# Optimization experiments

Hardware: AMD Instinct MI355X
Metric: run time of the kernel (lower is better)

The kernel has to match this reference:

```python
import jax, jax.numpy as jnp
import numpy as np

TAU = 2.0      # LIFNode default tau
VTH = 1.0      # v_threshold
ALPHA = 2.0    # ATan surrogate alpha
EPS = 1e-5     # BatchNorm eps
SCALE = 0.125  # hardcoded attention scale
HEADS = 8

@jax.custom_vjp
def atan_spike(x):
    return (x >= 0.0).astype(x.dtype)

def _atan_fwd(x):
    return atan_spike(x), x

def _atan_bwd(x, g):
    sg = (ALPHA / 2.0) / (1.0 + (jnp.pi / 2.0 * ALPHA * x) ** 2)
    return (g * sg,)

atan_spike.defvjp(_atan_fwd, _atan_bwd)

def lif(x_seq):
    # multi-step LIF: v' = v + (x - v)/tau ; spike = H(v'-1) ; hard reset to 0 (detach_reset)
    def step(v, x):
        v = v + (x - v) / TAU
        s = atan_spike(v - VTH)
        v = v * (1.0 - jax.lax.stop_gradient(s))
        return v, s
    _, spikes = jax.lax.scan(step, jnp.zeros_like(x_seq[0]), x_seq)
    return spikes

def bn(x, gamma, beta, mean, var):
    # inference-mode BatchNorm1d over channel axis 2 of [T,B,C,N]
    inv = gamma / jnp.sqrt(var + EPS)
    return x * inv[None, None, :, None] + (beta - mean * inv)[None, None, :, None]

def setup_inputs() -> dict:
    key = jax.random.key(0)
    ks = jax.random.split(key, 24)
    T, B, C, H, W = 4, 8, 512, 32, 32
    inp = {"x": jax.random.normal(ks[0], (T, B, C, H, W), dtype=jnp.float32)}
    i = 1
    for p in ("q", "k", "v", "proj"):
        inp[p + "_w"] = jax.random.normal(ks[i], (C, C), dtype=jnp.float32) / np.sqrt(C); i += 1
        inp[p + "_gamma"] = jax.random.uniform(ks[i], (C,), minval=0.5, maxval=1.5, dtype=jnp.float32); i += 1
        inp[p + "_beta"] = 0.1 * jax.random.normal(ks[i], (C,), dtype=jnp.float32); i += 1
        inp[p + "_mean"] = 0.1 * jax.random.normal(ks[i], (C,), dtype=jnp.float32); i += 1
        inp[p + "_var"] = jax.random.uniform(ks[i], (C,), minval=0.5, maxval=1.5, dtype=jnp.float32); i += 1
    inp["proj_b"] = 0.1 * jax.random.normal(ks[i], (C,), dtype=jnp.float32)
    return inp

def reference(x, q_w, q_gamma, q_beta, q_mean, q_var,
              k_w, k_gamma, k_beta, k_mean, k_var,
              v_w, v_gamma, v_beta, v_mean, v_var,
              proj_w, proj_gamma, proj_beta, proj_mean, proj_var, proj_b):
    T, B, C, H, W = x.shape
    N = H * W
    d = C // HEADS
    s = lif(x).reshape(T, B, C, N)  # proj_lif then flatten HW

    def branch(w, g, b, m, v_):
        y = jnp.einsum('oc,tbcn->tbon', w, s)  # conv1x1 == channel GEMM
        y = lif(bn(y, g, b, m, v_))
        # [T,B,C,N] -> [T,B,h,N,d]
        return y.reshape(T, B, HEADS, d, N).transpose(0, 1, 2, 4, 3)

    q = branch(q_w, q_gamma, q_beta, q_mean, q_var)
    k = branch(k_w, k_gamma, k_beta, k_mean, k_var)
    v = branch(v_w, v_gamma, v_beta, v_mean, v_var)

    kv = jnp.einsum('tbhnd,tbhne->tbhde', k, v)          # k^T v : [T,B,h,d,d]
    att = jnp.einsum('tbhnd,tbhde->tbhne', q, kv) * SCALE  # [T,B,h,N,d]
    att = att.transpose(0, 1, 2, 4, 3).reshape(T, B, C, N)
    a = lif(att)

    y = jnp.einsum('oc,tbcn->tbon', proj_w, a) + proj_b[None, None, :, None]
    y = bn(y, proj_gamma, proj_beta, proj_mean, proj_var)
    return y.reshape(T, B, C, H, W)
```

## Files before the change

### kernel.cpp

```cpp
#include <hip/hip_runtime.h>
#include <cstdint>
#include <cstddef>

typedef unsigned short u16;
typedef __attribute__((ext_vector_type(8))) short sh8;
typedef __attribute__((ext_vector_type(8))) _Float16 hf8;
typedef __attribute__((ext_vector_type(4))) float f4;

#define MFMA16B(a, b, c) __builtin_amdgcn_mfma_f32_16x16x32_bf16((a), (b), (c), 0, 0, 0)
#define MFMA16H(a, b, c) __builtin_amdgcn_mfma_f32_16x16x32_f16((a), (b), (c), 0, 0, 0)

__device__ __forceinline__ u16 f2bf(float f) {
  union { float f; uint32_t u; } v; v.f = f;
  uint32_t u = v.u;
  uint32_t lsb = (u >> 16) & 1u;
  return (u16)((u + 0x7fffu + lsb) >> 16);
}
__device__ __forceinline__ float bf2f(u16 h) {
  union { uint32_t u; float f; } v; v.u = ((uint32_t)h) << 16;
  return v.f;
}

__device__ __forceinline__ void aload16(const void* g, void* l) {
  __builtin_amdgcn_global_load_lds(
      (const __attribute__((address_space(1))) uint32_t*)g,
      (__attribute__((address_space(3))) uint32_t*)l, 16, 0, 0);
}

__global__ void prep_weights(const float* __restrict__ qw, const float* __restrict__ kw,
                             const float* __restrict__ vw, const float* __restrict__ pw,
                             u16* __restrict__ w2qkv, u16* __restrict__ w2p) {
  #pragma clang fp contract(off)
  int row = blockIdx.x;
  const float* src;
  u16* dst;
  int M, m;
  if (row < 1536) {
    int br = row >> 9;
    src = (br == 0 ? qw : (br == 1 ? kw : vw)) + (size_t)(row & 511) * 512;
    dst = w2qkv; M = 1536; m = row;
  } else {
    src = pw + (size_t)(row - 1536) * 512;
    dst = w2p; M = 512; m = row - 1536;
  }
  for (int c = threadIdx.x; c < 512; c += 256) {
    float w = src[c];
    _Float16 h0 = (_Float16)w;
    float r1 = w - (float)h0;
    _Float16 h1 = (_Float16)r1;
    union { _Float16 h; u16 u; } u0, u1;
    u0.h = h0; u1.h = h1;
    dst[(size_t)m * 512 + c] = u0.u;
    dst[(size_t)(M + m) * 512 + c] = u1.u;
  }
}

__global__ void bn_prep(const float* __restrict__ g, const float* __restrict__ be,
                        const float* __restrict__ mu, const float* __restrict__ va,
                        float* __restrict__ inv, float* __restrict__ add) {
  #pragma clang fp contract(off)
  int i = blockIdx.x * 256 + threadIdx.x;
  if (i < 512) {
    float iv = g[i] / sqrtf(va[i] + 1e-5f);
    inv[i] = iv;
    add[i] = be[i] - mu[i] * iv;
  }
}

__global__ __launch_bounds__(256) void lif0(const float* __restrict__ x, u16* __restrict__ sT) {
  #pragma clang fp contract(off)
  __shared__ u16 st[64 * 80];
  const int tid = threadIdx.x;
  const int n0 = blockIdx.x * 64;
  const int c0 = blockIdx.y * 64;
  const int b = blockIdx.z;
  const int cl = tid >> 2;
  const int ns = (tid & 3) * 16;
  const int nr = tid >> 2;
  const int cs = (tid & 3) * 16;
  float vv[16];
#pragma unroll
  for (int i = 0; i < 16; i++) vv[i] = 0.f;
  for (int t = 0; t < 4; ++t) {
    const float* xp = x + ((size_t)((t * 8 + b) * 512 + c0 + cl)) * 1024 + n0 + ns;
#pragma unroll
    for (int q = 0; q < 4; ++q) {
      f4 xv = *(const f4*)(xp + q * 4);
#pragma unroll
      for (int j = 0; j < 4; ++j) {
        int i = q * 4 + j;
        float v2 = vv[i] + (xv[j] - vv[i]) * 0.5f;
        int spk = (v2 - 1.0f >= 0.0f);
        st[(ns + i) * 80 + cl] = spk ? (u16)0x3C00 : (u16)0;
        vv[i] = spk ? 0.0f : v2;
      }
    }
    __syncthreads();
    u16* gp = sT + ((size_t)((t * 8 + b) * 1024 + n0 + nr)) * 512 + c0 + cs;
    *(sh8*)(gp) = *(const sh8*)&st[nr * 80 + cs];
    *(sh8*)(gp + 8) = *(const sh8*)&st[nr * 80 + cs + 8];
    __syncthreads();
  }
}

__global__ __launch_bounds__(256, 2) void qkv_gemm(
    const u16* __restrict__ w2, const u16* __restrict__ sT,
    const float* __restrict__ inv4, const float* __restrict__ add4,
    u16* __restrict__ qs, u16* __restrict__ ks, u16* __restrict__ vs) {
  #pragma clang fp contract(off)
  __shared__ u16 lA[2 * 128 * 32];
  __shared__ u16 lB[128 * 32];
  const int tid = threadIdx.x;
  const int m0 = blockIdx.x * 128;
  const int n0 = blockIdx.y * 128;
  const int b = blockIdx.z;
  const int branch = m0 >> 9;
  const int oc0 = m0 & 511;
  u16* dst = branch == 0 ? qs : (branch == 1 ? ks : vs);
  const int lane = tid & 63, wv = tid >> 6;
  const int l15 = lane & 15, l4 = lane >> 4;
  const int wm = wv >> 1, wn = wv & 1;
  const int rA = tid >> 2;
  const int kswz = (((tid & 3) ^ ((tid >> 3) & 3)) * 8);
  const int sA = (l4 ^ ((l15 >> 1) & 3)) * 8;

  size_t aoff[4];
#pragma unroll
  for (int c = 0; c < 4; ++c) {
    int rf = c * 64 + rA;
    int sp = rf >> 7, r = rf & 127;
    aoff[c] = (size_t)(sp * 1536 + m0 + r) * 512 + kswz;
  }
  size_t boff[2];
#pragma unroll
  for (int c = 0; c < 2; ++c) boff[c] = (size_t)(c * 64 + rA) * 512 + kswz;

  const f4 fz = {0.f, 0.f, 0.f, 0.f};
  f4 vst[4][4];
#pragma unroll
  for (int i = 0; i < 4; i++)
#pragma unroll
    for (int j = 0; j < 4; j++) vst[i][j] = fz;

  for (int t = 0; t < 4; ++t) {
    f4 acc[4][4];
#pragma unroll
    for (int i = 0; i < 4; i++)
#pragma unroll
      for (int j = 0; j < 4; j++) acc[i][j] = fz;
    const u16* sTt = sT + ((size_t)((t * 8 + b) * 1024 + n0)) * 512;

    for (int k0 = 0; k0 < 512; k0 += 32) {
#pragma unroll
      for (int c = 0; c < 4; ++c)
        aload16(w2 + aoff[c] + k0, &lA[c * 2048 + tid * 8]);
#pragma unroll
      for (int c = 0; c < 2; ++c)
        aload16(sTt + boff[c] + k0, &lB[c * 2048 + tid * 8]);
      __syncthreads();
      hf8 bfr[4];
#pragma unroll
      for (int nf = 0; nf < 4; ++nf)
        bfr[nf] = *(const hf8*)&lB[(wn * 64 + nf * 16 + l15) * 32 + sA];
#pragma unroll
      for (int sp = 0; sp < 2; ++sp) {
#pragma unroll
        for (int mf = 0; mf < 4; ++mf) {
          hf8 afr = *(const hf8*)&lA[sp * 4096 + (wm * 64 + mf * 16 + l15) * 32 + sA];
#pragma unroll
          for (int nf = 0; nf < 4; ++nf) acc[mf][nf] = MFMA16H(afr, bfr[nf], acc[mf][nf]);
        }
      }
      __syncthreads();
    }
#pragma unroll
    for (int mf = 0; mf < 4; ++mf) {
#pragma unroll
      for (int r = 0; r < 4; ++r) {
        int oc = oc0 + wm * 64 + mf * 16 + l4 * 4 + r;
        float iv = inv4[branch * 512 + oc];
        float ad = add4[branch * 512 + oc];
        size_t rowbase = ((size_t)((t * 8 + b) * 512 + oc)) * 1024 + n0;
#pragma unroll
        for (int nf = 0; nf < 4; ++nf) {
          float z = acc[mf][nf][r] * iv + ad;
          float v2 = vst[mf][nf][r];
          v2 = v2 + (z - v2) * 0.5f;
          int spk = (v2 - 1.0f >= 0.0f);
          vst[mf][nf][r] = spk ? 0.0f : v2;
          dst[rowbase + wn * 64 + nf * 16 + l15] = spk ? (u16)0x3F80 : (u16)0;
        }
      }
    }
  }
}

__global__ __launch_bounds__(256) void kv_gemm(const u16* __restrict__ ks,
                                               const u16* __restrict__ vs,
                                               float* __restrict__ kvp) {
  const int tbh = blockIdx.x;
  const int kc = blockIdx.y;
  const int tid = threadIdx.x;
  const int wv = tid >> 6, lane = tid & 63, l15 = lane & 15, l4 = lane >> 4;
  const size_t cb = ((size_t)(tbh >> 3) * 512 + (size_t)(tbh & 7) * 64) * 1024;
  const u16* vbase = vs + cb;
  const u16* kbase = ks + cb;
  const f4 fz = {0.f, 0.f, 0.f, 0.f};
  f4 acc[4];
#pragma unroll
  for (int i = 0; i < 4; i++) acc[i] = fz;
  for (int s = 0; s < 8; ++s) {
    int kk = kc * 256 + s * 32 + l4 * 8;
    sh8 av = *(const sh8*)(vbase + (size_t)(wv * 16 + l15) * 1024 + kk);
#pragma unroll
    for (int df = 0; df < 4; ++df) {
      sh8 bk = *(const sh8*)(kbase + (size_t)(df * 16 + l15) * 1024 + kk);
      acc[df] = MFMA16B(av, bk, acc[df]);
    }
  }
  float* out = kvp + ((size_t)kc * 256 + tbh) * 4096;
#pragma unroll
  for (int df = 0; df < 4; ++df)
#pragma unroll
    for (int r = 0; r < 4; ++r)
      out[(wv * 16 + l4 * 4 + r) * 64 + df * 16 + l15] = acc[df][r];
}

__global__ __launch_bounds__(256) void att_lif(const u16* __restrict__ qs,
                                               const float* __restrict__ kvp,
                                               u16* __restrict__ aT) {
  #pragma clang fp contract(off)
  __shared__ u16 ldsb[64 * 72 * 2 + 128 * 72];
  u16* lkhi = ldsb;
  u16* lklo = ldsb + 64 * 72;
  u16* lqT = ldsb + 64 * 72 * 2;
  u16* lsp = ldsb;
  const int tid = threadIdx.x;
  const int n0 = blockIdx.x * 128;
  const int b = blockIdx.y >> 3;
  const int h = blockIdx.y & 7;
  const int wv = tid >> 6, lane = tid & 63, l15 = lane & 15, l4 = lane >> 4;
  const int e_s = tid >> 2, ds_ = (tid & 3) * 16;
  const f4 fz = {0.f, 0.f, 0.f, 0.f};
  f4 vst[4][2];
#pragma unroll
  for (int i = 0; i < 4; i++)
#pragma unroll
    for (int j = 0; j < 2; j++) vst[i][j] = fz;

  for (int t = 0; t < 4; ++t) {
    int tb = t * 8 + b;
    int tbh = tb * 8 + h;
    {
      const float* base = kvp + (size_t)tbh * 4096 + e_s * 64 + ds_;
#pragma unroll
      for (int q = 0; q < 4; ++q) {
        f4 s4 = fz;
#pragma unroll
        for (int kc = 0; kc < 4; ++kc) s4 += *(const f4*)(base + (size_t)kc * 256 * 4096 + q * 4);
#pragma unroll
        for (int j = 0; j < 4; ++j) {
          float sv = s4[j];
          u16 hb = f2bf(sv);
          float lof = sv - bf2f(hb);
          lkhi[e_s * 72 + ds_ + q * 4 + j] = hb;
          lklo[e_s * 72 + ds_ + q * 4 + j] = f2bf(lof);
        }
      }
    }
    {
      const u16* qb = qs + ((size_t)tb * 512 + h * 64) * 1024 + n0;
#pragma unroll
      for (int it = 0; it < 4; ++it) {
        int lin = it * 2048 + tid * 8;
        int d = lin >> 7, j0 = lin & 127;
        sh8 qv = *(const sh8*)(qb + (size_t)d * 1024 + j0);
#pragma unroll
        for (int j = 0; j < 8; ++j) lqT[(j0 + j) * 72 + d] = (u16)qv[j];
      }
    }
    __syncthreads();
    f4 acc[4][2];
#pragma unroll
    for (int i = 0; i < 4; i++)
#pragma unroll
      for (int j = 0; j < 2; j++) acc[i][j] = fz;
#pragma unroll
    for (int ksx = 0; ksx < 2; ++ksx) {
      sh8 bq[2];
#pragma unroll
      for (int nf = 0; nf < 2; ++nf)
        bq[nf] = *(const sh8*)&lqT[(wv * 32 + nf * 16 + l15) * 72 + ksx * 32 + l4 * 8];
#pragma unroll
      for (int mf = 0; mf < 4; ++mf) {
        sh8 ah = *(const sh8*)&lkhi[(mf * 16 + l15) * 72 + ksx * 32 + l4 * 8];
        sh8 al = *(const sh8*)&lklo[(mf * 16 + l15) * 72 + ksx * 32 + l4 * 8];
#pragma unroll
        for (int nf = 0; nf < 2; ++nf) {
          acc[mf][nf] = MFMA16B(ah, bq[nf], acc[mf][nf]);
          acc[mf][nf] = MFMA16B(al, bq[nf], acc[mf][nf]);
        }
      }
    }
    __syncthreads();
#pragma unroll
    for (int mf = 0; mf < 4; ++mf)
#pragma unroll
      for (int nf = 0; nf < 2; ++nf)
#pragma unroll
        for (int r = 0; r < 4; ++r) {
          float xatt = acc[mf][nf][r] * 0.125f;
          float v2 = vst[mf][nf][r];
          v2 = v2 + (xatt - v2) * 0.5f;
          int spk = (v2 - 1.0f >= 0.0f);
          vst[mf][nf][r] = spk ? 0.0f : v2;
          int e = mf * 16 + l4 * 4 + r;
          int n = wv * 32 + nf * 16 + l15;
          lsp[n * 72 + e] = spk ? (u16)0x3C00 : (u16)0;
        }
    __syncthreads();
    {
#pragma unroll
      for (int it = 0; it < 2; ++it) {
        int lin = it * 256 + tid;
        int n = lin >> 2, es = (lin & 3) * 16;
        u16* gp = aT + ((size_t)(tb * 1024 + n0 + n)) * 512 + h * 64 + es;
        *(sh8*)gp = *(const sh8*)&lsp[n * 72 + es];
        *(sh8*)(gp + 8) = *(const sh8*)&lsp[n * 72 + es + 8];
      }
    }
    __syncthreads();
  }
}

__global__ __launch_bounds__(256, 2) void proj_gemm(
    const u16* __restrict__ w2, const u16* __restrict__ aT,
    const float* __restrict__ inv4, const float* __restrict__ add4,
    const float* __restrict__ pb, float* __restrict__ out) {
  #pragma clang fp contract(off)
  __shared__ u16 lA[2 * 128 * 32];
  __shared__ u16 lB[128 * 32];
  const int tid = threadIdx.x;
  const int m0 = blockIdx.x * 128;
  const int n0 = blockIdx.y * 128;
  const int tb = blockIdx.z;
  const int lane = tid & 63, wv = tid >> 6;
  const int l15 = lane & 15, l4 = lane >> 4;
  const int wm = wv >> 1, wn = wv & 1;
  const int rA = tid >> 2;
  const int kswz = (((tid & 3) ^ ((tid >> 3) & 3)) * 8);
  const int sA = (l4 ^ ((l15 >> 1) & 3)) * 8;

  size_t aoff[4];
#pragma unroll
  for (int c = 0; c < 4; ++c) {
    int rf = c * 64 + rA;
    int sp = rf >> 7, r = rf & 127;
    aoff[c] = (size_t)(sp * 512 + m0 + r) * 512 + kswz;
  }
  size_t boff[2];
#pragma unroll
  for (int c = 0; c < 2; ++c) boff[c] = (size_t)(c * 64 + rA) * 512 + kswz;

  const f4 fz = {0.f, 0.f, 0.f, 0.f};
  f4 acc[4][4];
#pragma unroll
  for (int i = 0; i < 4; i++)
#pragma unroll
    for (int j = 0; j < 4; j++) acc[i][j] = fz;
  const u16* aTt = aT + ((size_t)tb * 1024 + n0) * 512;

  for (int k0 = 0; k0 < 512; k0 += 32) {
#pragma unroll
    for (int c = 0; c < 4; ++c)
      aload16(w2 + aoff[c] + k0, &lA[c * 2048 + tid * 8]);
#pragma unroll
    for (int c = 0; c < 2; ++c)
      aload16(aTt + boff[c] + k0, &lB[c * 2048 + tid * 8]);
    __syncthreads();
    hf8 bfr[4];
#pragma unroll
    for (int nf = 0; nf < 4; ++nf)
      bfr[nf] = *(const hf8*)&lB[(wn * 64 + nf * 16 + l15) * 32 + sA];
#pragma unroll
    for (int sp = 0; sp < 2; ++sp) {
#pragma unroll
      for (int mf = 0; mf < 4; ++mf) {
        hf8 afr = *(const hf8*)&lA[sp * 4096 + (wm * 64 + mf * 16 + l15) * 32 + sA];
#pragma unroll
        for (int nf = 0; nf < 4; ++nf) acc[mf][nf] = MFMA16H(afr, bfr[nf], acc[mf][nf]);
      }
    }
    __syncthreads();
  }
#pragma unroll
  for (int mf = 0; mf < 4; ++mf) {
#pragma unroll
    for (int r = 0; r < 4; ++r) {
      int o = m0 + wm * 64 + mf * 16 + l4 * 4 + r;
      float iv = inv4[3 * 512 + o];
      float ad = add4[3 * 512 + o];
      float bias = pb[o];
      size_t rowbase = ((size_t)(tb * 512 + o)) * 1024 + n0;
#pragma unroll
      for (int nf = 0; nf < 4; ++nf) {
        float z = (acc[mf][nf][r] + bias) * iv + ad;
        out[rowbase + wn * 64 + nf * 16 + l15] = z;
      }
    }
  }
}

extern "C" void kernel_launch(void* const* d_in, const int* in_sizes, int n_in,
                              void* d_out, int out_size, void* d_ws, size_t ws_size,
                              hipStream_t stream) {
  const float* x = (const float*)d_in[0];
  const float* qw = (const float*)d_in[1];
  const float* kw = (const float*)d_in[6];
  const float* vw = (const float*)d_in[11];
  const float* pw = (const float*)d_in[16];
  const float* pb = (const float*)d_in[21];

  char* p = (char*)d_ws;
  u16* w2qkv = (u16*)p; p += (size_t)2 * 1536 * 512 * 2;
  u16* w2p = (u16*)p;   p += (size_t)2 * 512 * 512 * 2;
  float* inv4 = (float*)p; p += 4 * 512 * 4;
  float* add4 = (float*)p; p += 4 * 512 * 4;
  u16* sT = (u16*)p;    p += (size_t)4 * 8 * 1024 * 512 * 2;
  u16* qs = (u16*)p;    p += (size_t)4 * 8 * 512 * 1024 * 2;
  u16* ks = (u16*)p;    p += (size_t)4 * 8 * 512 * 1024 * 2;
  u16* vs = (u16*)p;    p += (size_t)4 * 8 * 512 * 1024 * 2;
  float* kvp = (float*)p; p += (size_t)4 * 256 * 4096 * 4;
  u16* aT = sT;
  float* out = (float*)d_out;

  prep_weights<<<dim3(2048), dim3(256), 0, stream>>>(qw, kw, vw, pw, w2qkv, w2p);
  for (int s = 0; s < 4; ++s) {
    const float* g  = (const float*)d_in[2 + s * 5];
    const float* be = (const float*)d_in[3 + s * 5];
    const float* mu = (const float*)d_in[4 + s * 5];
    const float* va = (const float*)d_in[5 + s * 5];
    bn_prep<<<dim3(2), dim3(256), 0, stream>>>(g, be, mu, va, inv4 + s * 512, add4 + s * 512);
  }
  lif0<<<dim3(16, 8, 8), dim3(256), 0, stream>>>(x, sT);
  qkv_gemm<<<dim3(12, 8, 8), dim3(256), 0, stream>>>(w2qkv, sT, inv4, add4, qs, ks, vs);
  kv_gemm<<<dim3(256, 4), dim3(256), 0, stream>>>(ks, vs, kvp);
  att_lif<<<dim3(8, 64), dim3(256), 0, stream>>>(qs, kvp, aT);
  proj_gemm<<<dim3(4, 8, 32), dim3(256), 0, stream>>>(w2p, aT, inv4, add4, pb, out);
}
```

Baseline: 265.0 us.

## Rewrite QKV GEMM with larger tiles, double-buffered LDS prefetch and XCD remap

The QKV GEMM now uses 512-thread blocks with 192x256 tiles and K=64 steps. LDS is double-buffered, and the next tile's async global-to-LDS loads are interleaved between MFMA quads with priority hints. The hi/lo fp16 weight split is laid out as one contiguous 1024-wide K row, and block IDs are remapped so tiles are grouped per chiplet. Separately, the KV GEMM drops its 4-way split-K and the partial-sum reduction in att_lif. This gives fewer, longer blocks, with a risk of lower parallelism there.

```diff
diff --git a/kernel.cpp b/kernel.cpp
--- a/kernel.cpp
+++ b/kernel.cpp
@@ -27,31 +27,55 @@
       (__attribute__((address_space(3))) uint32_t*)l, 16, 0, 0);
 }
 
+__device__ __forceinline__ void pbar() {
+  __builtin_amdgcn_sched_barrier(0);
+  __builtin_amdgcn_s_barrier();
+  __builtin_amdgcn_sched_barrier(0);
+}
+__device__ __forceinline__ void tile_bar() {
+  asm volatile("s_waitcnt vmcnt(0)" ::: "memory");
+  __builtin_amdgcn_s_barrier();
+  __builtin_amdgcn_sched_barrier(0);
+}
+
+#define QUAD12(Af, Bf, MH, NH)                                                \
+  {                                                                           \
+    __builtin_amdgcn_s_setprio(1);                                            \
+    _Pragma("unroll") for (int kk = 0; kk < 2; ++kk)                          \
+      _Pragma("unroll") for (int nf = 0; nf < 2; ++nf)                        \
+        _Pragma("unroll") for (int mf = 0; mf < 3; ++mf)                      \
+          acc[(MH)*3 + mf][(NH)*2 + nf] = MFMA16H(                            \
+              Af[mf][kk], Bf[nf][kk], acc[(MH)*3 + mf][(NH)*2 + nf]);         \
+    __builtin_amdgcn_s_setprio(0);                                            \
+  }
+
 __global__ void prep_weights(const float* __restrict__ qw, const float* __restrict__ kw,
                              const float* __restrict__ vw, const float* __restrict__ pw,
                              u16* __restrict__ w2qkv, u16* __restrict__ w2p) {
   #pragma clang fp contract(off)
   int row = blockIdx.x;
-  const float* src;
-  u16* dst;
-  int M, m;
-  if (row < 1536) {
-    int br = row >> 9;
-    src = (br == 0 ? qw : (br == 1 ? kw : vw)) + (size_t)(row & 511) * 512;
-    dst = w2qkv; M = 1536; m = row;
-  } else {
-    src = pw + (size_t)(row - 1536) * 512;
-    dst = w2p; M = 512; m = row - 1536;
-  }
   for (int c = threadIdx.x; c < 512; c += 256) {
+    const float* src;
+    if (row < 1536) {
+      int br = row >> 9;
+      src = (br == 0 ? qw : (br == 1 ? kw : vw)) + (size_t)(row & 511) * 512;
+    } else {
+      src = pw + (size_t)(row - 1536) * 512;
+    }
     float w = src[c];
     _Float16 h0 = (_Float16)w;
     float r1 = w - (float)h0;
     _Float16 h1 = (_Float16)r1;
     union { _Float16 h; u16 u; } u0, u1;
     u0.h = h0; u1.h = h1;
-    dst[(size_t)m * 512 + c] = u0.u;
-    dst[(size_t)(M + m) * 512 + c] = u1.u;
+    if (row < 1536) {
+      w2qkv[(size_t)row * 1024 + c] = u0.u;
+      w2qkv[(size_t)row * 1024 + 512 + c] = u1.u;
+    } else {
+      int m = row - 1536;
+      w2p[(size_t)m * 512 + c] = u0.u;
+      w2p[(size_t)(512 + m) * 512 + c] = u1.u;
+    }
   }
 }
 
@@ -103,83 +127,135 @@
   }
 }
 
-__global__ __launch_bounds__(256, 2) void qkv_gemm(
-    const u16* __restrict__ w2, const u16* __restrict__ sT,
+__global__ __launch_bounds__(512, 2) void qkv_gemm(
+    const u16* __restrict__ w2,
+    const u16* __restrict__ sT,
     const float* __restrict__ inv4, const float* __restrict__ add4,
     u16* __restrict__ qs, u16* __restrict__ ks, u16* __restrict__ vs) {
   #pragma clang fp contract(off)
-  __shared__ u16 lA[2 * 128 * 32];
-  __shared__ u16 lB[128 * 32];
+  __shared__ u16 lA[2][192 * 64];
+  __shared__ u16 lB[2][256 * 64];
   const int tid = threadIdx.x;
-  const int m0 = blockIdx.x * 128;
-  const int n0 = blockIdx.y * 128;
-  const int b = blockIdx.z;
-  const int branch = m0 >> 9;
-  const int oc0 = m0 & 511;
-  u16* dst = branch == 0 ? qs : (branch == 1 ? ks : vs);
-  const int lane = tid & 63, wv = tid >> 6;
+  const int bid = blockIdx.x;
+  const int orig = (bid & 7) * 32 + (bid >> 3);
+  const int mI = orig & 7;
+  const int nI = (orig >> 3) & 3;
+  const int b  = orig >> 5;
+  const int m0 = mI * 192;
+  const int n0 = nI * 256;
+  const int wid = tid >> 6, lane = tid & 63;
   const int l15 = lane & 15, l4 = lane >> 4;
-  const int wm = wv >> 1, wn = wv & 1;
-  const int rA = tid >> 2;
-  const int kswz = (((tid & 3) ^ ((tid >> 3) & 3)) * 8);
-  const int sA = (l4 ^ ((l15 >> 1) & 3)) * 8;
-
-  size_t aoff[4];
-#pragma unroll
-  for (int c = 0; c < 4; ++c) {
-    int rf = c * 64 + rA;
-    int sp = rf >> 7, r = rf & 127;
-    aoff[c] = (size_t)(sp * 1536 + m0 + r) * 512 + kswz;
-  }
-  size_t boff[2];
-#pragma unroll
-  for (int c = 0; c < 2; ++c) boff[c] = (size_t)(c * 64 + rA) * 512 + kswz;
+  const int wm = wid >> 2, wn = wid & 3;
+  const int srow = tid >> 3;
+  const int sslot = (tid & 7) ^ (srow & 7);
+  int aoff[3];
+#pragma unroll
+  for (int c = 0; c < 3; ++c)
+    aoff[c] = (m0 + c * 64 + srow) * 1024 + sslot * 8;
+  int boff[4];
+#pragma unroll
+  for (int c = 0; c < 4; ++c)
+    boff[c] = (n0 + c * 64 + srow) * 512 + sslot * 8;
+
+  auto stA = [&](int bf, int ii) {
+    int k0 = (ii & 15) * 64;
+#pragma unroll
+    for (int c = 0; c < 3; ++c)
+      aload16(w2 + (size_t)aoff[c] + k0, &lA[bf][c * 4096 + tid * 8]);
+  };
+  auto stB = [&](int bf, int ii, int c0) {
+    int bk0 = (ii & 7) * 64;
+    int tt = ii >> 4;
+    const u16* bb = sT + (size_t)tt * 4194304 + (size_t)b * 524288;
+#pragma unroll
+    for (int c = c0; c < c0 + 2; ++c)
+      aload16(bb + (size_t)boff[c] + bk0, &lB[bf][c * 4096 + tid * 8]);
+  };
 
   const f4 fz = {0.f, 0.f, 0.f, 0.f};
-  f4 vst[4][4];
-#pragma unroll
-  for (int i = 0; i < 4; i++)
+  f4 acc[6][4];
+  f4 vst[6][4];
+#pragma unroll
+  for (int i = 0; i < 6; i++)
 #pragma unroll
     for (int j = 0; j < 4; j++) vst[i][j] = fz;
 
+  stA(0, 0); stB(0, 0, 0); stB(0, 0, 2);
+  tile_bar();
+  int buf = 0;
+
   for (int t = 0; t < 4; ++t) {
-    f4 acc[4][4];
-#pragma unroll
-    for (int i = 0; i < 4; i++)
+#pragma unroll
+    for (int i = 0; i < 6; i++)
 #pragma unroll
       for (int j = 0; j < 4; j++) acc[i][j] = fz;
-    const u16* sTt = sT + ((size_t)((t * 8 + b) * 1024 + n0)) * 512;
-
-    for (int k0 = 0; k0 < 512; k0 += 32) {
-#pragma unroll
-      for (int c = 0; c < 4; ++c)
-        aload16(w2 + aoff[c] + k0, &lA[c * 2048 + tid * 8]);
-#pragma unroll
-      for (int c = 0; c < 2; ++c)
-        aload16(sTt + boff[c] + k0, &lB[c * 2048 + tid * 8]);
-      __syncthreads();
-      hf8 bfr[4];
-#pragma unroll
-      for (int nf = 0; nf < 4; ++nf)
-        bfr[nf] = *(const hf8*)&lB[(wn * 64 + nf * 16 + l15) * 32 + sA];
-#pragma unroll
-      for (int sp = 0; sp < 2; ++sp) {
-#pragma unroll
-        for (int mf = 0; mf < 4; ++mf) {
-          hf8 afr = *(const hf8*)&lA[sp * 4096 + (wm * 64 + mf * 16 + l15) * 32 + sA];
-#pragma unroll
-          for (int nf = 0; nf < 4; ++nf) acc[mf][nf] = MFMA16H(afr, bfr[nf], acc[mf][nf]);
-        }
-      }
-      __syncthreads();
-    }
-#pragma unroll
-    for (int mf = 0; mf < 4; ++mf) {
+
+    for (int i = 0; i < 16; ++i) {
+      const int ii = t * 16 + i;
+      const bool pf = (ii < 63);
+      hf8 A0[3][2], Bq[2][2];
+#pragma unroll
+      for (int mf = 0; mf < 3; ++mf)
+#pragma unroll
+        for (int kk = 0; kk < 2; ++kk) {
+          int lr = wm * 96 + mf * 16 + l15;
+          A0[mf][kk] = *(const hf8*)&lA[buf][lr * 64 + (((kk * 4 + l4) ^ (l15 & 7)) * 8)];
+        }
+#pragma unroll
+      for (int nf = 0; nf < 2; ++nf)
+#pragma unroll
+        for (int kk = 0; kk < 2; ++kk) {
+          int lr = wn * 64 + nf * 16 + l15;
+          Bq[nf][kk] = *(const hf8*)&lB[buf][lr * 64 + (((kk * 4 + l4) ^ (l15 & 7)) * 8)];
+        }
+      if (pf) stA(buf ^ 1, ii + 1);
+      pbar();
+      QUAD12(A0, Bq, 0, 0);
+      hf8 B1[2][2];
+#pragma unroll
+      for (int nf = 0; nf < 2; ++nf)
+#pragma unroll
+        for (int kk = 0; kk < 2; ++kk) {
+          int lr = wn * 64 + (2 + nf) * 16 + l15;
+          B1[nf][kk] = *(const hf8*)&lB[buf][lr * 64 + (((kk * 4 + l4) ^ (l15 & 7)) * 8)];
+        }
+      if (pf) stB(buf ^ 1, ii + 1, 0);
+      pbar();
+      QUAD12(A0, B1, 0, 1);
+      hf8 A1[3][2];
+#pragma unroll
+      for (int mf = 0; mf < 3; ++mf)
+#pragma unroll
+        for (int kk = 0; kk < 2; ++kk) {
+          int lr = wm * 96 + (3 + mf) * 16 + l15;
+          A1[mf][kk] = *(const hf8*)&lA[buf][lr * 64 + (((kk * 4 + l4) ^ (l15 & 7)) * 8)];
+        }
+      if (pf) stB(buf ^ 1, ii + 1, 2);
+      pbar();
+      QUAD12(A1, B1, 1, 1);
+#pragma unroll
+      for (int nf = 0; nf < 2; ++nf)
+#pragma unroll
+        for (int kk = 0; kk < 2; ++kk) {
+          int lr = wn * 64 + nf * 16 + l15;
+          Bq[nf][kk] = *(const hf8*)&lB[buf][lr * 64 + (((kk * 4 + l4) ^ (l15 & 7)) * 8)];
+        }
+      pbar();
+      QUAD12(A1, Bq, 1, 0);
+      tile_bar();
+      buf ^= 1;
+    }
+#pragma unroll
+    for (int mf = 0; mf < 6; ++mf) {
+      int f0 = m0 + wm * 96 + mf * 16;
+      int br = f0 >> 9;
+      u16* dst = br == 0 ? qs : (br == 1 ? ks : vs);
+      int ocb = f0 & 511;
 #pragma unroll
       for (int r = 0; r < 4; ++r) {
-        int oc = oc0 + wm * 64 + mf * 16 + l4 * 4 + r;
-        float iv = inv4[branch * 512 + oc];
-        float ad = add4[branch * 512 + oc];
+        int oc = ocb + l4 * 4 + r;
+        float iv = inv4[br * 512 + oc];
+        float ad = add4[br * 512 + oc];
         size_t rowbase = ((size_t)((t * 8 + b) * 512 + oc)) * 1024 + n0;
 #pragma unroll
         for (int nf = 0; nf < 4; ++nf) {
@@ -199,7 +275,6 @@
                                                const u16* __restrict__ vs,
                                                float* __restrict__ kvp) {
   const int tbh = blockIdx.x;
-  const int kc = blockIdx.y;
   const int tid = threadIdx.x;
   const int wv = tid >> 6, lane = tid & 63, l15 = lane & 15, l4 = lane >> 4;
   const size_t cb = ((size_t)(tbh >> 3) * 512 + (size_t)(tbh & 7) * 64) * 1024;
@@ -209,8 +284,8 @@
   f4 acc[4];
 #pragma unroll
   for (int i = 0; i < 4; i++) acc[i] = fz;
-  for (int s = 0; s < 8; ++s) {
-    int kk = kc * 256 + s * 32 + l4 * 8;
+  for (int s = 0; s < 32; ++s) {
+    int kk = s * 32 + l4 * 8;
     sh8 av = *(const sh8*)(vbase + (size_t)(wv * 16 + l15) * 1024 + kk);
 #pragma unroll
     for (int df = 0; df < 4; ++df) {
@@ -218,7 +293,7 @@
       acc[df] = MFMA16B(av, bk, acc[df]);
     }
   }
-  float* out = kvp + ((size_t)kc * 256 + tbh) * 4096;
+  float* out = kvp + (size_t)tbh * 4096;
 #pragma unroll
   for (int df = 0; df < 4; ++df)
 #pragma unroll
@@ -255,9 +330,7 @@
       const float* base = kvp + (size_t)tbh * 4096 + e_s * 64 + ds_;
 #pragma unroll
       for (int q = 0; q < 4; ++q) {
-        f4 s4 = fz;
-#pragma unroll
-        for (int kc = 0; kc < 4; ++kc) s4 += *(const f4*)(base + (size_t)kc * 256 * 4096 + q * 4);
+        f4 s4 = *(const f4*)(base + q * 4);
 #pragma unroll
         for (int j = 0; j < 4; ++j) {
           float sv = s4[j];
@@ -422,7 +495,7 @@
   const float* pb = (const float*)d_in[21];
 
   char* p = (char*)d_ws;
-  u16* w2qkv = (u16*)p; p += (size_t)2 * 1536 * 512 * 2;
+  u16* w2qkv = (u16*)p; p += (size_t)1536 * 1024 * 2;
   u16* w2p = (u16*)p;   p += (size_t)2 * 512 * 512 * 2;
   float* inv4 = (float*)p; p += 4 * 512 * 4;
   float* add4 = (float*)p; p += 4 * 512 * 4;
@@ -430,7 +503,7 @@
   u16* qs = (u16*)p;    p += (size_t)4 * 8 * 512 * 1024 * 2;
   u16* ks = (u16*)p;    p += (size_t)4 * 8 * 512 * 1024 * 2;
   u16* vs = (u16*)p;    p += (size_t)4 * 8 * 512 * 1024 * 2;
-  float* kvp = (float*)p; p += (size_t)4 * 256 * 4096 * 4;
+  float* kvp = (float*)p; p += (size_t)256 * 4096 * 4;
   u16* aT = sT;
   float* out = (float*)d_out;
 
@@ -443,8 +516,8 @@
     bn_prep<<<dim3(2), dim3(256), 0, stream>>>(g, be, mu, va, inv4 + s * 512, add4 + s * 512);
   }
   lif0<<<dim3(16, 8, 8), dim3(256), 0, stream>>>(x, sT);
-  qkv_gemm<<<dim3(12, 8, 8), dim3(256), 0, stream>>>(w2qkv, sT, inv4, add4, qs, ks, vs);
-  kv_gemm<<<dim3(256, 4), dim3(256), 0, stream>>>(ks, vs, kvp);
+  qkv_gemm<<<dim3(256), dim3(512), 0, stream>>>(w2qkv, sT, inv4, add4, qs, ks, vs);
+  kv_gemm<<<dim3(256), dim3(256), 0, stream>>>(ks, vs, kvp);
   att_lif<<<dim3(8, 64), dim3(256), 0, stream>>>(qs, kvp, aT);
   proj_gemm<<<dim3(4, 8, 32), dim3(256), 0, stream>>>(w2p, aT, inv4, add4, pb, out);
 }
```

Result: faster. 251.6 us (-5.0%).
